# Kernel tuning notes

Measured on AMD Instinct MI355X. Metric: run time of the kernel, lower is better.

Reference implementation:

```python
import jax, jax.numpy as jnp
import numpy as np

IN_FEATURES = 4096
OUT_FEATURES = 11008

def setup_inputs() -> dict:
    key = jax.random.key(0)
    k_x, k_w, k_s, k_b = jax.random.split(key, 4)
    x = jax.random.normal(k_x, (4, 2048, IN_FEATURES), dtype=jnp.float32)
    # int8 quantized weight, stored [out_features, in_features] as in torch
    weight = jax.random.randint(k_w, (OUT_FEATURES, IN_FEATURES), -128, 128, dtype=jnp.int8)
    scales = jax.random.uniform(k_s, (OUT_FEATURES,), dtype=jnp.float32, minval=0.005, maxval=0.02)
    bias = jax.random.normal(k_b, (OUT_FEATURES,), dtype=jnp.float32) * 0.02
    return {"x": x, "weight": weight, "scales": scales, "bias": bias}

def reference(x, weight, scales, bias):
    # F.linear(x, weight.to(x.dtype)) * scales + bias
    w = weight.astype(x.dtype)               # [O, I] dequant-to-activation-dtype (scale applied post-matmul)
    y = jnp.einsum('bsi,oi->bso', x, w)      # [B, S, O]
    return y * scales + bias
```

## Files before the change

kernel.cpp:

```cpp
#include <hip/hip_runtime.h>
#include <hip/hip_bf16.h>
#include <stdint.h>

#define M_DIM 8192
#define K_DIM 4096
#define N_DIM 11008
#define BM 128
#define BN 128
#define BK 64

typedef __bf16 bf16x8 __attribute__((ext_vector_type(8)));
typedef float f32x4 __attribute__((ext_vector_type(4)));
typedef short short8 __attribute__((ext_vector_type(8)));

__device__ __forceinline__ ushort f32_to_bf16_rne(float f) {
    uint32_t u = __builtin_bit_cast(uint32_t, f);
    return (ushort)((u + 0x7fffu + ((u >> 16) & 1u)) >> 16);
}

__global__ __launch_bounds__(256) void cvt_x_kernel(const float* __restrict__ x,
                                                    ushort* __restrict__ o, int n8) {
    int t = blockIdx.x * 256 + threadIdx.x;
    if (t >= n8) return;
    const float4* src = (const float4*)x + (size_t)t * 2;
    float4 a = src[0], b = src[1];
    union { ushort u[8]; short8 v; } r;
    r.u[0] = f32_to_bf16_rne(a.x); r.u[1] = f32_to_bf16_rne(a.y);
    r.u[2] = f32_to_bf16_rne(a.z); r.u[3] = f32_to_bf16_rne(a.w);
    r.u[4] = f32_to_bf16_rne(b.x); r.u[5] = f32_to_bf16_rne(b.y);
    r.u[6] = f32_to_bf16_rne(b.z); r.u[7] = f32_to_bf16_rne(b.w);
    *(short8*)(o + (size_t)t * 8) = r.v;
}

__global__ __launch_bounds__(256) void cvt_w_kernel(const int* __restrict__ w,
                                                    ushort* __restrict__ o, int n8) {
    int t = blockIdx.x * 256 + threadIdx.x;
    if (t >= n8) return;
    const int4* src = (const int4*)w + (size_t)t * 2;
    int4 a = src[0], b = src[1];
    union { ushort u[8]; short8 v; } r;
    r.u[0] = f32_to_bf16_rne((float)a.x); r.u[1] = f32_to_bf16_rne((float)a.y);
    r.u[2] = f32_to_bf16_rne((float)a.z); r.u[3] = f32_to_bf16_rne((float)a.w);
    r.u[4] = f32_to_bf16_rne((float)b.x); r.u[5] = f32_to_bf16_rne((float)b.y);
    r.u[6] = f32_to_bf16_rne((float)b.z); r.u[7] = f32_to_bf16_rne((float)b.w);
    *(short8*)(o + (size_t)t * 8) = r.v;
}

__global__ __launch_bounds__(256) void gemm_bf16_kernel(
    const ushort* __restrict__ A, const ushort* __restrict__ B,
    const float* __restrict__ scales, const float* __restrict__ bias,
    float* __restrict__ out) {
    __shared__ ushort sA[BM * BK];
    __shared__ ushort sB[BN * BK];

    const int t = threadIdx.x;
    const int l = t & 63;
    const int w = t >> 6;
    const int wm = w >> 1, wn = w & 1;

    const int m0 = blockIdx.y * BM;
    const int n0 = blockIdx.x * BN;

    const int r_base = t >> 3;
    const int g = (t & 7) ^ (r_base & 7);
    const ushort* aSrc = A + (size_t)(m0 + r_base) * K_DIM + g * 8;
    const ushort* bSrc = B + (size_t)(n0 + r_base) * K_DIM + g * 8;

    const int rowA = wm * 64 + (l & 15);
    const int rowB = wn * 64 + (l & 15);
    const int colg0 = (((l >> 4)) ^ (l & 7)) * 8;
    const int colg1 = (((l >> 4) + 4) ^ (l & 7)) * 8;

    f32x4 acc[4][4] = {};

    for (int kt = 0; kt < K_DIM / BK; ++kt) {
        const int k0 = kt * BK;
        __syncthreads();
#pragma unroll
        for (int i = 0; i < 4; ++i) {
            __builtin_amdgcn_global_load_lds(
                (__attribute__((address_space(1))) void*)(aSrc + (size_t)i * 32 * K_DIM + k0),
                (__attribute__((address_space(3))) void*)(sA + i * 2048 + w * 512),
                16, 0, 0);
        }
#pragma unroll
        for (int i = 0; i < 4; ++i) {
            __builtin_amdgcn_global_load_lds(
                (__attribute__((address_space(1))) void*)(bSrc + (size_t)i * 32 * K_DIM + k0),
                (__attribute__((address_space(3))) void*)(sB + i * 2048 + w * 512),
                16, 0, 0);
        }
        __syncthreads();

#pragma unroll
        for (int ks = 0; ks < 2; ++ks) {
            const int cg = ks ? colg1 : colg0;
            bf16x8 af[4], bfr[4];
#pragma unroll
            for (int i = 0; i < 4; ++i)
                af[i] = *(const bf16x8*)(sA + (rowA + i * 16) * 64 + cg);
#pragma unroll
            for (int j = 0; j < 4; ++j)
                bfr[j] = *(const bf16x8*)(sB + (rowB + j * 16) * 64 + cg);
#pragma unroll
            for (int i = 0; i < 4; ++i)
#pragma unroll
                for (int j = 0; j < 4; ++j)
                    acc[i][j] = __builtin_amdgcn_mfma_f32_16x16x32_bf16(
                        af[i], bfr[j], acc[i][j], 0, 0, 0);
        }
    }

    const int mrow = m0 + wm * 64 + (l >> 4) * 4;
    const int ncol = n0 + wn * 64 + (l & 15);
#pragma unroll
    for (int j = 0; j < 4; ++j) {
        const int n = ncol + j * 16;
        const float s = scales[n];
        const float bz = bias[n];
#pragma unroll
        for (int i = 0; i < 4; ++i) {
            const int m = mrow + i * 16;
#pragma unroll
            for (int r2 = 0; r2 < 4; ++r2) {
                out[(size_t)(m + r2) * N_DIM + n] = acc[i][j][r2] * s + bz;
            }
        }
    }
}

extern "C" void kernel_launch(void* const* d_in, const int* in_sizes, int n_in,
                              void* d_out, int out_size, void* d_ws, size_t ws_size,
                              hipStream_t stream) {
    const float* x = (const float*)d_in[0];
    const int* wq = (const int*)d_in[1];
    const float* scales = (const float*)d_in[2];
    const float* bias = (const float*)d_in[3];
    float* out = (float*)d_out;

    const size_t x_elems = (size_t)M_DIM * K_DIM;
    const size_t w_elems = (size_t)N_DIM * K_DIM;
    const size_t need = (x_elems + w_elems) * sizeof(ushort);
    if (ws_size < need) return;

    ushort* xb = (ushort*)d_ws;
    ushort* wb = xb + x_elems;

    cvt_x_kernel<<<dim3((int)(x_elems / 8 / 256)), dim3(256), 0, stream>>>(x, xb, (int)(x_elems / 8));
    cvt_w_kernel<<<dim3((int)(w_elems / 8 / 256)), dim3(256), 0, stream>>>(wq, wb, (int)(w_elems / 8));

    gemm_bf16_kernel<<<dim3(N_DIM / BN, M_DIM / BM), dim3(256), 0, stream>>>(
        xb, wb, scales, bias, out);
}
```

Before: 1.539 ms.

## Rewrite GEMM as 256x256 double-buffered 8-wave pipeline with XCD-aware block swizzle

Replaces the 128x128 single-buffered GEMM with a 256x256 tile per 512-thread block and double-buffered LDS. Each K-step is split into four quarter phases that interleave async global-to-LDS staging of the next tiles with MFMA work, using barriers, explicit waitcnt and s_setprio. It also remaps the 1D grid so consecutive blocks spread across XCDs while sharing A/B tiles. The goal is to hide global-load latency and raise arithmetic intensity, at the cost of more registers and LDS (128 KB per block) and fragile hand-tuned waitcnt counts.

```diff
diff --git a/kernel.cpp b/kernel.cpp
--- a/kernel.cpp
+++ b/kernel.cpp
@@ -5,9 +5,10 @@
 #define M_DIM 8192
 #define K_DIM 4096
 #define N_DIM 11008
-#define BM 128
-#define BN 128
+#define BM 256
+#define BN 256
 #define BK 64
+#define NKT (K_DIM / BK)
 
 typedef __bf16 bf16x8 __attribute__((ext_vector_type(8)));
 typedef float f32x4 __attribute__((ext_vector_type(4)));
@@ -46,84 +47,166 @@
     *(short8*)(o + (size_t)t * 8) = r.v;
 }
 
-__global__ __launch_bounds__(256) void gemm_bf16_kernel(
+__global__ __launch_bounds__(512, 2) void gemm_bf16_kernel(
     const ushort* __restrict__ A, const ushort* __restrict__ B,
     const float* __restrict__ scales, const float* __restrict__ bias,
     float* __restrict__ out) {
-    __shared__ ushort sA[BM * BK];
-    __shared__ ushort sB[BN * BK];
+    __shared__ ushort sA[2 * BM * BK];
+    __shared__ ushort sB[2 * BN * BK];
 
     const int t = threadIdx.x;
     const int l = t & 63;
     const int w = t >> 6;
-    const int wm = w >> 1, wn = w & 1;
-
-    const int m0 = blockIdx.y * BM;
-    const int n0 = blockIdx.x * BN;
-
-    const int r_base = t >> 3;
-    const int g = (t & 7) ^ (r_base & 7);
-    const ushort* aSrc = A + (size_t)(m0 + r_base) * K_DIM + g * 8;
-    const ushort* bSrc = B + (size_t)(n0 + r_base) * K_DIM + g * 8;
-
-    const int rowA = wm * 64 + (l & 15);
-    const int rowB = wn * 64 + (l & 15);
-    const int colg0 = (((l >> 4)) ^ (l & 7)) * 8;
-    const int colg1 = (((l >> 4) + 4) ^ (l & 7)) * 8;
-
-    f32x4 acc[4][4] = {};
-
-    for (int kt = 0; kt < K_DIM / BK; ++kt) {
-        const int k0 = kt * BK;
-        __syncthreads();
+    const int wm = w >> 2;
+    const int wn = w & 3;
+
+    const int bid = blockIdx.x;
+    const int sw = (bid & 7) * 172 + (bid >> 3);
+    const int bn = sw % 43;
+    const int bm = sw / 43;
+    const int m0 = bm * BM;
+    const int n0 = bn * BN;
+
+    const int r8 = t >> 3;
+    const int gsw = (t & 7) ^ (r8 & 7);
+    const ushort* aSrc = A + (size_t)(m0 + r8) * K_DIM + gsw * 8;
+    const ushort* bSrc = B + (size_t)(n0 + r8) * K_DIM + gsw * 8;
+    const int ldsW = w * 512;
+
+    const int rowA = wm * 128 + (l & 15);
+    const int rowB = wn * 32 + (l & 15);
+    const int cg0 = (((l >> 4) + 0) ^ (l & 7)) * 8;
+    const int cg1 = (((l >> 4) + 4) ^ (l & 7)) * 8;
+
+    bf16x8 af[8];
+    bf16x8 blo[4];
+    bf16x8 bhi[4];
+    f32x4 acc[8][4] = {};
+
+#define STAGE(SRC, DST, H, KT, BUFO)                                              \
+    do {                                                                          \
+        const ushort* _s = (SRC) + (size_t)((H) * 128) * K_DIM + (KT) * BK;       \
+        ushort* _d = (DST) + (BUFO) + (H) * 8192 + ldsW;                          \
+        __builtin_amdgcn_global_load_lds(                                         \
+            (__attribute__((address_space(1))) void*)_s,                          \
+            (__attribute__((address_space(3))) void*)_d, 16, 0, 0);               \
+        __builtin_amdgcn_global_load_lds(                                         \
+            (__attribute__((address_space(1))) void*)(_s + (size_t)64 * K_DIM),   \
+            (__attribute__((address_space(3))) void*)(_d + 4096), 16, 0, 0);      \
+    } while (0)
+
+#define TILE_BODY(T, CB)                                                            \
+    do {                                                                            \
+        const int _k1 = ((T) + 1 < NKT) ? (T) + 1 : NKT - 1;                        \
+        const int _k2 = ((T) + 2 < NKT) ? (T) + 2 : NKT - 1;                        \
+        const int _cb = (CB) * (BM * BK);                                           \
+             \
+        _Pragma("unroll") for (int mf = 0; mf < 4; ++mf) {                          \
+            af[mf * 2 + 0] = *(const bf16x8*)(sA + _cb + (rowA + mf * 16) * BK + cg0); \
+            af[mf * 2 + 1] = *(const bf16x8*)(sA + _cb + (rowA + mf * 16) * BK + cg1); \
+        }                                                                           \
+        _Pragma("unroll") for (int nf = 0; nf < 2; ++nf) {                          \
+            blo[nf * 2 + 0] = *(const bf16x8*)(sB + _cb + (rowB + nf * 16) * BK + cg0); \
+            blo[nf * 2 + 1] = *(const bf16x8*)(sB + _cb + (rowB + nf * 16) * BK + cg1); \
+        }                                                                           \
+        STAGE(aSrc, sA, 1, _k1, ((CB) ^ 1) * (BM * BK));                            \
+        __builtin_amdgcn_s_barrier();                                               \
+        asm volatile("s_waitcnt lgkmcnt(0)" ::: "memory");                          \
+        __builtin_amdgcn_s_setprio(1);                                              \
+        _Pragma("unroll") for (int mf = 0; mf < 4; ++mf)                            \
+        _Pragma("unroll") for (int nf = 0; nf < 2; ++nf) {                          \
+            acc[mf][nf] = __builtin_amdgcn_mfma_f32_16x16x32_bf16(                  \
+                af[mf * 2 + 0], blo[nf * 2 + 0], acc[mf][nf], 0, 0, 0);             \
+            acc[mf][nf] = __builtin_amdgcn_mfma_f32_16x16x32_bf16(                  \
+                af[mf * 2 + 1], blo[nf * 2 + 1], acc[mf][nf], 0, 0, 0);             \
+        }                                                                           \
+        __builtin_amdgcn_s_setprio(0);                                              \
+        __builtin_amdgcn_s_barrier();                                               \
+                     \
+        _Pragma("unroll") for (int nf = 0; nf < 2; ++nf) {                          \
+            bhi[nf * 2 + 0] = *(const bf16x8*)(sB + _cb + (rowB + 128 + nf * 16) * BK + cg0); \
+            bhi[nf * 2 + 1] = *(const bf16x8*)(sB + _cb + (rowB + 128 + nf * 16) * BK + cg1); \
+        }                                                                           \
+        STAGE(bSrc, sB, 0, _k2, (CB) * (BM * BK));                                  \
+        __builtin_amdgcn_s_barrier();                                               \
+        asm volatile("s_waitcnt lgkmcnt(0)" ::: "memory");                          \
+        __builtin_amdgcn_s_setprio(1);                                              \
+        _Pragma("unroll") for (int mf = 0; mf < 4; ++mf)                            \
+        _Pragma("unroll") for (int nf = 0; nf < 2; ++nf) {                          \
+            acc[mf][nf + 2] = __builtin_amdgcn_mfma_f32_16x16x32_bf16(              \
+                af[mf * 2 + 0], bhi[nf * 2 + 0], acc[mf][nf + 2], 0, 0, 0);         \
+            acc[mf][nf + 2] = __builtin_amdgcn_mfma_f32_16x16x32_bf16(              \
+                af[mf * 2 + 1], bhi[nf * 2 + 1], acc[mf][nf + 2], 0, 0, 0);         \
+        }                                                                           \
+        __builtin_amdgcn_s_setprio(0);                                              \
+        __builtin_amdgcn_s_barrier();                                               \
+        \
+        _Pragma("unroll") for (int mf = 0; mf < 4; ++mf) {                          \
+            af[mf * 2 + 0] = *(const bf16x8*)(sA + _cb + (rowA + (mf + 4) * 16) * BK + cg0); \
+            af[mf * 2 + 1] = *(const bf16x8*)(sA + _cb + (rowA + (mf + 4) * 16) * BK + cg1); \
+        }                                                                           \
+        STAGE(bSrc, sB, 1, _k2, (CB) * (BM * BK));                                  \
+        __builtin_amdgcn_s_barrier();                                               \
+        asm volatile("s_waitcnt lgkmcnt(0)" ::: "memory");                          \
+        __builtin_amdgcn_s_setprio(1);                                              \
+        _Pragma("unroll") for (int mf = 0; mf < 4; ++mf)                            \
+        _Pragma("unroll") for (int nf = 0; nf < 2; ++nf) {                          \
+            acc[mf + 4][nf] = __builtin_amdgcn_mfma_f32_16x16x32_bf16(              \
+                af[mf * 2 + 0], blo[nf * 2 + 0], acc[mf + 4][nf], 0, 0, 0);         \
+            acc[mf + 4][nf] = __builtin_amdgcn_mfma_f32_16x16x32_bf16(              \
+                af[mf * 2 + 1], blo[nf * 2 + 1], acc[mf + 4][nf], 0, 0, 0);         \
+        }                                                                           \
+        __builtin_amdgcn_s_setprio(0);                                              \
+        __builtin_amdgcn_s_barrier();                                               \
+           \
+        STAGE(aSrc, sA, 0, _k2, (CB) * (BM * BK));                                  \
+        asm volatile("s_waitcnt vmcnt(6)" ::: "memory");                            \
+        __builtin_amdgcn_s_barrier();                                               \
+        __builtin_amdgcn_s_setprio(1);                                              \
+        _Pragma("unroll") for (int mf = 0; mf < 4; ++mf)                            \
+        _Pragma("unroll") for (int nf = 0; nf < 2; ++nf) {                          \
+            acc[mf + 4][nf + 2] = __builtin_amdgcn_mfma_f32_16x16x32_bf16(          \
+                af[mf * 2 + 0], bhi[nf * 2 + 0], acc[mf + 4][nf + 2], 0, 0, 0);     \
+            acc[mf + 4][nf + 2] = __builtin_amdgcn_mfma_f32_16x16x32_bf16(          \
+                af[mf * 2 + 1], bhi[nf * 2 + 1], acc[mf + 4][nf + 2], 0, 0, 0);     \
+        }                                                                           \
+        __builtin_amdgcn_s_setprio(0);                                              \
+        __builtin_amdgcn_s_barrier();                                               \
+    } while (0)
+
+    STAGE(aSrc, sA, 0, 0, 0);
+    STAGE(aSrc, sA, 1, 0, 0);
+    STAGE(bSrc, sB, 0, 0, 0);
+    STAGE(bSrc, sB, 1, 0, 0);
+    STAGE(bSrc, sB, 0, 1, BM * BK);
+    STAGE(bSrc, sB, 1, 1, BM * BK);
+    STAGE(aSrc, sA, 0, 1, BM * BK);
+    asm volatile("s_waitcnt vmcnt(6)" ::: "memory");
+    __builtin_amdgcn_s_barrier();
+
+    for (int kt = 0; kt < NKT; kt += 2) {
+        TILE_BODY(kt, 0);
+        TILE_BODY(kt + 1, 1);
+    }
+
+#undef TILE_BODY
+#undef STAGE
+
+    asm volatile("s_waitcnt vmcnt(0)" ::: "memory");
+
+    const int mBase = m0 + wm * 128 + (l >> 4) * 4;
+    const int nBase = n0 + wn * 32 + (l & 15);
 #pragma unroll
-        for (int i = 0; i < 4; ++i) {
-            __builtin_amdgcn_global_load_lds(
-                (__attribute__((address_space(1))) void*)(aSrc + (size_t)i * 32 * K_DIM + k0),
-                (__attribute__((address_space(3))) void*)(sA + i * 2048 + w * 512),
-                16, 0, 0);
-        }
-#pragma unroll
-        for (int i = 0; i < 4; ++i) {
-            __builtin_amdgcn_global_load_lds(
-                (__attribute__((address_space(1))) void*)(bSrc + (size_t)i * 32 * K_DIM + k0),
-                (__attribute__((address_space(3))) void*)(sB + i * 2048 + w * 512),
-                16, 0, 0);
-        }
-        __syncthreads();
-
-#pragma unroll
-        for (int ks = 0; ks < 2; ++ks) {
-            const int cg = ks ? colg1 : colg0;
-            bf16x8 af[4], bfr[4];
-#pragma unroll
-            for (int i = 0; i < 4; ++i)
-                af[i] = *(const bf16x8*)(sA + (rowA + i * 16) * 64 + cg);
-#pragma unroll
-            for (int j = 0; j < 4; ++j)
-                bfr[j] = *(const bf16x8*)(sB + (rowB + j * 16) * 64 + cg);
-#pragma unroll
-            for (int i = 0; i < 4; ++i)
-#pragma unroll
-                for (int j = 0; j < 4; ++j)
-                    acc[i][j] = __builtin_amdgcn_mfma_f32_16x16x32_bf16(
-                        af[i], bfr[j], acc[i][j], 0, 0, 0);
-        }
-    }
-
-    const int mrow = m0 + wm * 64 + (l >> 4) * 4;
-    const int ncol = n0 + wn * 64 + (l & 15);
-#pragma unroll
-    for (int j = 0; j < 4; ++j) {
-        const int n = ncol + j * 16;
+    for (int nf = 0; nf < 4; ++nf) {
+        const int n = nBase + (nf & 1) * 16 + (nf >> 1) * 128;
         const float s = scales[n];
         const float bz = bias[n];
 #pragma unroll
-        for (int i = 0; i < 4; ++i) {
-            const int m = mrow + i * 16;
+        for (int mf = 0; mf < 8; ++mf) {
+            const int m = mBase + mf * 16;
 #pragma unroll
             for (int r2 = 0; r2 < 4; ++r2) {
-                out[(size_t)(m + r2) * N_DIM + n] = acc[i][j][r2] * s + bz;
+                out[(size_t)(m + r2) * N_DIM + n] = acc[mf][nf][r2] * s + bz;
             }
         }
     }
@@ -149,6 +232,6 @@
     cvt_x_kernel<<<dim3((int)(x_elems / 8 / 256)), dim3(256), 0, stream>>>(x, xb, (int)(x_elems / 8));
     cvt_w_kernel<<<dim3((int)(w_elems / 8 / 256)), dim3(256), 0, stream>>>(wq, wb, (int)(w_elems / 8));
 
-    gemm_bf16_kernel<<<dim3(N_DIM / BN, M_DIM / BM), dim3(256), 0, stream>>>(
+    gemm_bf16_kernel<<<dim3((N_DIM / BN) * (M_DIM / BM)), dim3(512), 0, stream>>>(
         xb, wb, scales, bias, out);
 }
```

After: 1.247 ms. 19.0% less time.
